# Performance work log

Measured on AMD Instinct MI355X. Metric: run time of the kernel, lower is better.

Reference implementation:

```python
import jax, jax.numpy as jnp
import numpy as np

N_NODES = 50000
N_EDGES = 800000
IN_DIM = 32
EMBED_DIM = 64
OUT_DIM = 1
N_LAYERS = 8


def setup_inputs() -> dict:
    key = jax.random.key(0)
    ks = jax.random.split(key, 10)
    x = jax.random.normal(ks[0], (N_NODES, IN_DIM), dtype=jnp.float32)
    src = jax.random.randint(ks[1], (N_EDGES,), 0, N_NODES, dtype=jnp.int32)
    dst = jax.random.randint(ks[2], (N_EDGES,), 0, N_NODES, dtype=jnp.int32)
    # learned params
    s_in = 1.0 / np.sqrt(IN_DIM)
    s_d = 1.0 / np.sqrt(EMBED_DIM)
    W_embed = jax.random.uniform(ks[3], (IN_DIM, EMBED_DIM), jnp.float32, -s_in, s_in)
    b_embed = jnp.zeros((EMBED_DIM,), jnp.float32)
    Ws = jax.random.uniform(ks[4], (N_LAYERS, EMBED_DIM, EMBED_DIM), jnp.float32, -s_d, s_d)
    bs = jnp.zeros((N_LAYERS, EMBED_DIM), jnp.float32)
    W_dec = jax.random.uniform(ks[5], (EMBED_DIM, OUT_DIM), jnp.float32, -s_d, s_d)
    b_dec = jnp.zeros((OUT_DIM,), jnp.float32)
    return {"x": x, "src": src, "dst": dst, "W_embed": W_embed, "b_embed": b_embed,
            "Ws": Ws, "bs": bs, "W_dec": W_dec, "b_dec": b_dec}


def reference(x, src, dst, W_embed, b_embed, Ws, bs, W_dec, b_dec):
    N = x.shape[0]
    ones = jnp.ones(src.shape[0], x.dtype)
    # DGL GraphConv norm='both': degrees clamped to min 1
    deg_out = jnp.maximum(jax.ops.segment_sum(ones, src, num_segments=N), 1.0)
    deg_in = jnp.maximum(jax.ops.segment_sum(ones, dst, num_segments=N), 1.0)
    inv_out = deg_out ** -0.5  # [N]
    inv_in = deg_in ** -0.5    # [N]

    h = x @ W_embed + b_embed  # [N, D]

    def layer(h, wb):
        W, b = wb
        m = (h * inv_out[:, None])[src]                      # gather [E, D]
        agg = jax.ops.segment_sum(m, dst, num_segments=N)    # scatter-add [N, D]
        h = (agg * inv_in[:, None]) @ W + b
        return h, None

    h, _ = jax.lax.scan(layer, h, (Ws, bs))
    return h @ W_dec + b_dec  # [N, OUT_DIM]
```

## Files before the change

kernel.cpp:

```cpp
#include <hip/hip_runtime.h>


#define PAD 48
#define HS 32
#define HR 4
#define HBLK (HS * HR)

__global__ __launch_bounds__(256) void prep_hist_kernel(
        const int* __restrict__ src,
        const float* __restrict__ W_embed, const float* __restrict__ b_embed,
        const float* __restrict__ Ws, const float* __restrict__ bs,
        const float* __restrict__ W_dec, float* __restrict__ coef,
        int* __restrict__ cursor, unsigned* __restrict__ pu, int N, int E) {
    __shared__ unsigned lds[8192];
    int b = blockIdx.x;
    if (b < HBLK) {
        int q = b >> 2, r = b & 3;
        for (int i = threadIdx.x; i < 8192; i += 256) lds[i] = 0;
        __syncthreads();
        int base = r << 14;
        int per = ((E + HS - 1) / HS + 3) & ~3;
        int e0 = q * per;
        int e1 = e0 + per; if (e1 > E) e1 = E;
        if (e0 < e1) {
            const int4* p4 = (const int4*)(src + e0);
            int m4 = (e1 - e0) >> 2;
            for (int i = threadIdx.x; i < m4; i += 256) {
                int4 v = p4[i];
                int t;
                t = v.x - base; if ((unsigned)t < 16384u) atomicAdd(&lds[t >> 1], 1u << ((t & 1) * 16));
                t = v.y - base; if ((unsigned)t < 16384u) atomicAdd(&lds[t >> 1], 1u << ((t & 1) * 16));
                t = v.z - base; if ((unsigned)t < 16384u) atomicAdd(&lds[t >> 1], 1u << ((t & 1) * 16));
                t = v.w - base; if ((unsigned)t < 16384u) atomicAdd(&lds[t >> 1], 1u << ((t & 1) * 16));
            }
            for (int e = e0 + (m4 << 2) + threadIdx.x; e < e1; e += 256) {
                int t = src[e] - base;
                if ((unsigned)t < 16384u) atomicAdd(&lds[t >> 1], 1u << ((t & 1) * 16));
            }
        }
        __syncthreads();
        unsigned* outp = pu + (size_t)b * 8192;
        for (int i = threadIdx.x; i < 8192; i += 256) outp[i] = lds[i];
    } else if (b == HBLK) {
        __shared__ float shv[64];
        __shared__ float shg[9];
        int i = threadIdx.x;
        if (i < 64) shv[i] = W_dec[i];
        __syncthreads();
        for (int l = 7; l >= 0; --l) {
            float a = 0.f;
            if (i < 64) {
                float p = bs[l * 64 + i] * shv[i];
                for (int d = 32; d; d >>= 1) p += __shfl_xor(p, d);
                if (i == 0) shg[l + 1] = p;
                const float* Wrow = Ws + l * 4096 + i * 64;
                for (int j = 0; j < 64; ++j) a += Wrow[j] * shv[j];
            }
            __syncthreads();
            if (i < 64) shv[i] = a;
            __syncthreads();
        }
        if (i < 64) {
            float p = b_embed[i] * shv[i];
            for (int d = 32; d; d >>= 1) p += __shfl_xor(p, d);
            if (i == 0) shg[0] = p;
        }
        __syncthreads();
        if (i < 32) {
            float a = 0.f;
            const float* Wr = W_embed + i * 64;
            for (int j = 0; j < 64; ++j) a += Wr[j] * shv[j];
            coef[16 + i] = a;
        }
        if (i < 9) coef[i] = shg[i];
    } else {
        int g = (b - HBLK - 1) * 256 + threadIdx.x;
        int stride = (gridDim.x - HBLK - 1) * 256;
        for (int i = g; i < N; i += stride) cursor[i] = 0;
    }
}

__global__ __launch_bounds__(256) void fill_kernel(
        const int* __restrict__ src, const int* __restrict__ dst,
        int* __restrict__ cursor, unsigned short* __restrict__ csr, int E) {
    int i = blockIdx.x * 256 + threadIdx.x;
    if (i >= E) return;
    int s = src[i], d = dst[i];
    int p = atomicAdd(&cursor[d], 1);
    if (p < PAD) csr[(size_t)d * PAD + p] = (unsigned short)s;
}

__global__ __launch_bounds__(256) void z0_kernel(
        const float* __restrict__ x, const float* __restrict__ coef,
        const unsigned* __restrict__ pu, const int* __restrict__ cursor,
        float* __restrict__ inv_out, float* __restrict__ inv_in,
        float* __restrict__ ts0, int N) {
    __shared__ float w[33];
    if (threadIdx.x < 32) w[threadIdx.x] = coef[16 + threadIdx.x];
    if (threadIdx.x == 32) w[32] = coef[0];
    __syncthreads();
    int n = blockIdx.x * 256 + threadIdx.x;
    if (n >= N) return;
    const float4* xr = (const float4*)(x + (size_t)n * 32);
    float acc = 0.f;
#pragma unroll
    for (int q = 0; q < 8; ++q) {
        float4 vv = xr[q];
        acc += vv.x * w[q * 4] + vv.y * w[q * 4 + 1] + vv.z * w[q * 4 + 2] + vv.w * w[q * 4 + 3];
    }
    int r = n >> 14, j = (n & 16383) >> 1, sh = (n & 1) * 16;
    int co = 0;
#pragma unroll
    for (int q = 0; q < HS; ++q)
        co += (pu[(size_t)((q << 2) | r) * 8192 + j] >> sh) & 0xFFFF;
    if (co < 1) co = 1;
    int ci = cursor[n]; if (ci < 1) ci = 1;
    float io = rsqrtf((float)co);
    inv_out[n] = io;
    inv_in[n] = rsqrtf((float)ci);
    ts0[n] = io * (acc + w[32]);
}

__device__ __forceinline__ float quad_gather(const unsigned short* __restrict__ row,
                                             const float* __restrict__ ta,
                                             int c, int sub) {
    float acc = 0.f;
#pragma unroll
    for (int t = 0; t < PAD / 16; ++t) {
        int eb = sub * 4 + 16 * t;
        if (eb < c) {
            uint2 v = *(const uint2*)(row + eb);
            unsigned i0 = v.x & 0xFFFF, i1 = v.x >> 16;
            unsigned i2 = v.y & 0xFFFF, i3 = v.y >> 16;
            acc += ta[i0];
            if (eb + 1 < c) acc += ta[i1];
            if (eb + 2 < c) acc += ta[i2];
            if (eb + 3 < c) acc += ta[i3];
        }
    }
    return acc;
}

__global__ __launch_bounds__(256) void prop_kernel(
        const float* __restrict__ ts_in, float* __restrict__ ts_out,
        const float* __restrict__ inv_out, const float* __restrict__ inv_in,
        const int* __restrict__ cursor, const unsigned short* __restrict__ csr,
        const float* __restrict__ coef, int k, int N) {
    int tid = blockIdx.x * 256 + threadIdx.x;
    int n = tid >> 2, sub = tid & 3;
    if (n >= N) return;
    int c = cursor[n]; if (c > PAD) c = PAD;
    float acc = quad_gather(csr + (size_t)n * PAD, ts_in, c, sub);
    acc += __shfl_xor(acc, 1);
    acc += __shfl_xor(acc, 2);
    if (sub == 0) ts_out[n] = inv_out[n] * (inv_in[n] * acc + coef[k]);
}

__global__ __launch_bounds__(256) void final_kernel(
        const float* __restrict__ ts_in, float* __restrict__ out,
        const float* __restrict__ inv_in, const int* __restrict__ cursor,
        const unsigned short* __restrict__ csr, const float* __restrict__ coef,
        const float* __restrict__ b_dec, int N) {
    int tid = blockIdx.x * 256 + threadIdx.x;
    int n = tid >> 2, sub = tid & 3;
    if (n >= N) return;
    int c = cursor[n]; if (c > PAD) c = PAD;
    float acc = quad_gather(csr + (size_t)n * PAD, ts_in, c, sub);
    acc += __shfl_xor(acc, 1);
    acc += __shfl_xor(acc, 2);
    if (sub == 0) out[n] = inv_in[n] * acc + coef[8] + b_dec[0];
}

__global__ __launch_bounds__(256) void prep_kernel_i(
        const float* __restrict__ W_embed, const float* __restrict__ b_embed,
        const float* __restrict__ Ws, const float* __restrict__ bs,
        const float* __restrict__ W_dec, float* __restrict__ coef,
        int* __restrict__ cnt, int NZ) {
    int g = blockIdx.x * 256 + threadIdx.x;
    for (int i = g; i < NZ; i += gridDim.x * 256) cnt[i] = 0;
    if (blockIdx.x == 0) {
        __shared__ float shv[64];
        __shared__ float shg[9];
        int i = threadIdx.x;
        if (i < 64) shv[i] = W_dec[i];
        __syncthreads();
        for (int l = 7; l >= 0; --l) {
            float a = 0.f;
            if (i < 64) {
                float p = bs[l * 64 + i] * shv[i];
                for (int d = 32; d; d >>= 1) p += __shfl_xor(p, d);
                if (i == 0) shg[l + 1] = p;
                const float* Wrow = Ws + l * 4096 + i * 64;
                for (int j = 0; j < 64; ++j) a += Wrow[j] * shv[j];
            }
            __syncthreads();
            if (i < 64) shv[i] = a;
            __syncthreads();
        }
        if (i < 64) {
            float p = b_embed[i] * shv[i];
            for (int d = 32; d; d >>= 1) p += __shfl_xor(p, d);
            if (i == 0) shg[0] = p;
        }
        __syncthreads();
        if (i < 32) {
            float a = 0.f;
            const float* Wr = W_embed + i * 64;
            for (int j = 0; j < 64; ++j) a += Wr[j] * shv[j];
            coef[16 + i] = a;
        }
        if (i < 9) coef[i] = shg[i];
    }
}

__global__ __launch_bounds__(256) void fill_kernel_i(
        const int* __restrict__ src, const int* __restrict__ dst,
        int* __restrict__ cnt_out, int* __restrict__ cursor,
        int* __restrict__ csr, int E) {
    int i = blockIdx.x * 256 + threadIdx.x;
    if (i >= E) return;
    int s = src[i], d = dst[i];
    atomicAdd(&cnt_out[s], 1);
    int p = atomicAdd(&cursor[d], 1);
    if (p < PAD) csr[(size_t)d * PAD + p] = s;
}

__global__ __launch_bounds__(256) void z0_kernel_i(
        const float* __restrict__ x, const float* __restrict__ coef,
        const int* __restrict__ cnt_out, const int* __restrict__ cursor,
        float* __restrict__ inv_out, float* __restrict__ inv_in,
        float* __restrict__ ts0, int N) {
    __shared__ float w[33];
    if (threadIdx.x < 32) w[threadIdx.x] = coef[16 + threadIdx.x];
    if (threadIdx.x == 32) w[32] = coef[0];
    __syncthreads();
    int n = blockIdx.x * 256 + threadIdx.x;
    if (n >= N) return;
    const float4* xr = (const float4*)(x + (size_t)n * 32);
    float acc = 0.f;
#pragma unroll
    for (int q = 0; q < 8; ++q) {
        float4 vv = xr[q];
        acc += vv.x * w[q * 4] + vv.y * w[q * 4 + 1] + vv.z * w[q * 4 + 2] + vv.w * w[q * 4 + 3];
    }
    int co = cnt_out[n]; if (co < 1) co = 1;
    int ci = cursor[n];  if (ci < 1) ci = 1;
    float io = rsqrtf((float)co);
    inv_out[n] = io;
    inv_in[n] = rsqrtf((float)ci);
    ts0[n] = io * (acc + w[32]);
}

__global__ __launch_bounds__(256) void prop_kernel_i(
        const float* __restrict__ ts_in, float* __restrict__ ts_out,
        const float* __restrict__ inv_out, const float* __restrict__ inv_in,
        const int* __restrict__ cursor, const int* __restrict__ csr,
        const float* __restrict__ coef, int k, int N) {
    int n = blockIdx.x * 256 + threadIdx.x;
    if (n >= N) return;
    int c = cursor[n]; if (c > PAD) c = PAD;
    const int* row = csr + (size_t)n * PAD;
    float acc = 0.f;
    for (int e = 0; e < c; ++e) acc += ts_in[row[e]];
    ts_out[n] = inv_out[n] * (inv_in[n] * acc + coef[k]);
}

__global__ __launch_bounds__(256) void final_kernel_i(
        const float* __restrict__ ts_in, float* __restrict__ out,
        const float* __restrict__ inv_in, const int* __restrict__ cursor,
        const int* __restrict__ csr, const float* __restrict__ coef,
        const float* __restrict__ b_dec, int N) {
    int n = blockIdx.x * 256 + threadIdx.x;
    if (n >= N) return;
    int c = cursor[n]; if (c > PAD) c = PAD;
    const int* row = csr + (size_t)n * PAD;
    float acc = 0.f;
    for (int e = 0; e < c; ++e) acc += ts_in[row[e]];
    out[n] = inv_in[n] * acc + coef[8] + b_dec[0];
}

extern "C" void kernel_launch(void* const* d_in, const int* in_sizes, int n_in,
                              void* d_out, int out_size, void* d_ws, size_t ws_size,
                              hipStream_t stream) {
    const float* x       = (const float*)d_in[0];
    const int*   src     = (const int*)d_in[1];
    const int*   dst     = (const int*)d_in[2];
    const float* W_embed = (const float*)d_in[3];
    const float* b_embed = (const float*)d_in[4];
    const float* Ws      = (const float*)d_in[5];
    const float* bs      = (const float*)d_in[6];
    const float* W_dec   = (const float*)d_in[7];
    const float* b_dec   = (const float*)d_in[8];
    float* out = (float*)d_out;
    int N = in_sizes[0] / 32;
    int E = in_sizes[1];

    char* w = (char*)d_ws;
    size_t o = 0;
    int* cursor = (int*)(w + o); o += (size_t)N * 4;
    size_t region = (size_t)HBLK * 8192 * 4;
    if ((size_t)N * 4 > region) region = (size_t)N * 4;
    unsigned* pu  = (unsigned*)(w + o);
    int* cnt_out  = (int*)(w + o);
    o += region; o = (o + 255) & ~(size_t)255;
    float* inv_out = (float*)(w + o); o += (size_t)N * 4; o = (o + 255) & ~(size_t)255;
    float* inv_in  = (float*)(w + o); o += (size_t)N * 4; o = (o + 255) & ~(size_t)255;
    float* coef    = (float*)(w + o); o += 256;
    float* tsA     = (float*)(w + o); o += (size_t)N * 4; o = (o + 255) & ~(size_t)255;
    float* tsB     = (float*)(w + o); o += (size_t)N * 4; o = (o + 255) & ~(size_t)255;
    void* csr_mem  = (void*)(w + o);

    int nbl  = (N + 255) / 256;
    int nbl4 = (4 * N + 255) / 256;
    int ebl  = (E + 255) / 256;

    if (N <= 65536) {
        unsigned short* csr = (unsigned short*)csr_mem;
        prep_hist_kernel<<<HBLK + 1 + 31, 256, 0, stream>>>(src, W_embed, b_embed, Ws, bs,
                                                            W_dec, coef, cursor, pu, N, E);
        fill_kernel<<<ebl, 256, 0, stream>>>(src, dst, cursor, csr, E);
        z0_kernel<<<nbl, 256, 0, stream>>>(x, coef, pu, cursor, inv_out, inv_in, tsA, N);
        float* ta = tsA; float* tb = tsB;
        for (int k = 1; k <= 7; ++k) {
            prop_kernel<<<nbl4, 256, 0, stream>>>(ta, tb, inv_out, inv_in, cursor, csr, coef, k, N);
            float* tmp = ta; ta = tb; tb = tmp;
        }
        final_kernel<<<nbl4, 256, 0, stream>>>(ta, out, inv_in, cursor, csr, coef, b_dec, N);
    } else {
        int* csr = (int*)csr_mem;
        prep_kernel_i<<<128, 256, 0, stream>>>(W_embed, b_embed, Ws, bs, W_dec, coef, cursor, 2 * N);
        fill_kernel_i<<<ebl, 256, 0, stream>>>(src, dst, cnt_out, cursor, csr, E);
        z0_kernel_i<<<nbl, 256, 0, stream>>>(x, coef, cnt_out, cursor, inv_out, inv_in, tsA, N);
        float* ta = tsA; float* tb = tsB;
        for (int k = 1; k <= 7; ++k) {
            prop_kernel_i<<<nbl, 256, 0, stream>>>(ta, tb, inv_out, inv_in, cursor, csr, coef, k, N);
            float* tmp = ta; ta = tb; tb = tmp;
        }
        final_kernel_i<<<nbl, 256, 0, stream>>>(ta, out, inv_in, cursor, csr, coef, b_dec, N);
    }
}
```

Baseline: 118.3 us.

## Replace global-atomic CSR fill with LDS-histogram based per-range slot assignment

```diff
diff --git a/kernel.cpp b/kernel.cpp
--- a/kernel.cpp
+++ b/kernel.cpp
@@ -2,46 +2,55 @@
 
 
 #define PAD 48
-#define HS 32
-#define HR 4
-#define HBLK (HS * HR)
+#define RS  8192
+#define RH  (RS / 2)
+#define QS  8
+#define QF  16
 
 __global__ __launch_bounds__(256) void prep_hist_kernel(
-        const int* __restrict__ src,
+        const int* __restrict__ src, const int* __restrict__ dst,
         const float* __restrict__ W_embed, const float* __restrict__ b_embed,
         const float* __restrict__ Ws, const float* __restrict__ bs,
         const float* __restrict__ W_dec, float* __restrict__ coef,
-        int* __restrict__ cursor, unsigned* __restrict__ pu, int N, int E) {
-    __shared__ unsigned lds[8192];
+        unsigned* __restrict__ pu_src, unsigned* __restrict__ pu_dst,
+        int NR, int N, int E) {
+    __shared__ unsigned lds[RH];
     int b = blockIdx.x;
-    if (b < HBLK) {
-        int q = b >> 2, r = b & 3;
-        for (int i = threadIdx.x; i < 8192; i += 256) lds[i] = 0;
-        __syncthreads();
-        int base = r << 14;
-        int per = ((E + HS - 1) / HS + 3) & ~3;
+    int nsrc = NR * QS;
+    int nhist = nsrc + NR * QF;
+    if (b < nhist) {
+        bool is_src = b < nsrc;
+        int bb = is_src ? b : b - nsrc;
+        int r = bb % NR, q = bb / NR;
+        int Q = is_src ? QS : QF;
+        const int* __restrict__ arr = is_src ? src : dst;
+        unsigned* __restrict__ pu = is_src ? pu_src : pu_dst;
+        for (int i = threadIdx.x; i < RH; i += 256) lds[i] = 0;
+        __syncthreads();
+        int base = r * RS;
+        int per = ((E + Q - 1) / Q + 3) & ~3;
         int e0 = q * per;
         int e1 = e0 + per; if (e1 > E) e1 = E;
-        if (e0 < e1) {
-            const int4* p4 = (const int4*)(src + e0);
+        if (e0 < E) {
+            const int4* p4 = (const int4*)(arr + e0);
             int m4 = (e1 - e0) >> 2;
             for (int i = threadIdx.x; i < m4; i += 256) {
                 int4 v = p4[i];
                 int t;
-                t = v.x - base; if ((unsigned)t < 16384u) atomicAdd(&lds[t >> 1], 1u << ((t & 1) * 16));
-                t = v.y - base; if ((unsigned)t < 16384u) atomicAdd(&lds[t >> 1], 1u << ((t & 1) * 16));
-                t = v.z - base; if ((unsigned)t < 16384u) atomicAdd(&lds[t >> 1], 1u << ((t & 1) * 16));
-                t = v.w - base; if ((unsigned)t < 16384u) atomicAdd(&lds[t >> 1], 1u << ((t & 1) * 16));
+                t = v.x - base; if ((unsigned)t < (unsigned)RS) atomicAdd(&lds[t >> 1], 1u << ((t & 1) * 16));
+                t = v.y - base; if ((unsigned)t < (unsigned)RS) atomicAdd(&lds[t >> 1], 1u << ((t & 1) * 16));
+                t = v.z - base; if ((unsigned)t < (unsigned)RS) atomicAdd(&lds[t >> 1], 1u << ((t & 1) * 16));
+                t = v.w - base; if ((unsigned)t < (unsigned)RS) atomicAdd(&lds[t >> 1], 1u << ((t & 1) * 16));
             }
             for (int e = e0 + (m4 << 2) + threadIdx.x; e < e1; e += 256) {
-                int t = src[e] - base;
-                if ((unsigned)t < 16384u) atomicAdd(&lds[t >> 1], 1u << ((t & 1) * 16));
-            }
-        }
-        __syncthreads();
-        unsigned* outp = pu + (size_t)b * 8192;
-        for (int i = threadIdx.x; i < 8192; i += 256) outp[i] = lds[i];
-    } else if (b == HBLK) {
+                int t = arr[e] - base;
+                if ((unsigned)t < (unsigned)RS) atomicAdd(&lds[t >> 1], 1u << ((t & 1) * 16));
+            }
+        }
+        __syncthreads();
+        unsigned* outp = pu + (size_t)(q * NR + r) * RH;
+        for (int i = threadIdx.x; i < RH; i += 256) outp[i] = lds[i];
+    } else if (b == nhist) {
         __shared__ float shv[64];
         __shared__ float shg[9];
         int i = threadIdx.x;
@@ -73,28 +82,79 @@
             coef[16 + i] = a;
         }
         if (i < 9) coef[i] = shg[i];
-    } else {
-        int g = (b - HBLK - 1) * 256 + threadIdx.x;
-        int stride = (gridDim.x - HBLK - 1) * 256;
-        for (int i = g; i < N; i += stride) cursor[i] = 0;
     }
 }
 
 __global__ __launch_bounds__(256) void fill_kernel(
         const int* __restrict__ src, const int* __restrict__ dst,
-        int* __restrict__ cursor, unsigned short* __restrict__ csr, int E) {
-    int i = blockIdx.x * 256 + threadIdx.x;
-    if (i >= E) return;
-    int s = src[i], d = dst[i];
-    int p = atomicAdd(&cursor[d], 1);
-    if (p < PAD) csr[(size_t)d * PAD + p] = (unsigned short)s;
+        const unsigned* __restrict__ pu_dst, unsigned* __restrict__ cnt_in,
+        unsigned short* __restrict__ csr, int NR, int E) {
+    __shared__ unsigned cur[RH];
+    int b = blockIdx.x;
+    int r = b % NR, q = b / NR;
+    for (int j = threadIdx.x; j < RH; j += 256) {
+        unsigned s = 0;
+        for (int qq = 0; qq < q; ++qq) s += pu_dst[(size_t)(qq * NR + r) * RH + j];
+        cur[j] = s;
+    }
+    __syncthreads();
+    int base = r * RS;
+    int per = ((E + QF - 1) / QF + 3) & ~3;
+    int e0 = q * per;
+    int e1 = e0 + per; if (e1 > E) e1 = E;
+    if (e0 < E) {
+        const int4* s4p = (const int4*)(src + e0);
+        const int4* d4p = (const int4*)(dst + e0);
+        int m4 = (e1 - e0) >> 2;
+        for (int i = threadIdx.x; i < m4; i += 256) {
+            int4 sv = s4p[i];
+            int4 dv = d4p[i];
+            int t, sh, p; unsigned old;
+            t = dv.x - base;
+            if ((unsigned)t < (unsigned)RS) {
+                sh = (t & 1) * 16; old = atomicAdd(&cur[t >> 1], 1u << sh);
+                p = (old >> sh) & 0xFFFF;
+                if (p < PAD) csr[(size_t)(base + t) * PAD + p] = (unsigned short)sv.x;
+            }
+            t = dv.y - base;
+            if ((unsigned)t < (unsigned)RS) {
+                sh = (t & 1) * 16; old = atomicAdd(&cur[t >> 1], 1u << sh);
+                p = (old >> sh) & 0xFFFF;
+                if (p < PAD) csr[(size_t)(base + t) * PAD + p] = (unsigned short)sv.y;
+            }
+            t = dv.z - base;
+            if ((unsigned)t < (unsigned)RS) {
+                sh = (t & 1) * 16; old = atomicAdd(&cur[t >> 1], 1u << sh);
+                p = (old >> sh) & 0xFFFF;
+                if (p < PAD) csr[(size_t)(base + t) * PAD + p] = (unsigned short)sv.z;
+            }
+            t = dv.w - base;
+            if ((unsigned)t < (unsigned)RS) {
+                sh = (t & 1) * 16; old = atomicAdd(&cur[t >> 1], 1u << sh);
+                p = (old >> sh) & 0xFFFF;
+                if (p < PAD) csr[(size_t)(base + t) * PAD + p] = (unsigned short)sv.w;
+            }
+        }
+        for (int e = e0 + (m4 << 2) + threadIdx.x; e < e1; e += 256) {
+            int t = dst[e] - base;
+            if ((unsigned)t < (unsigned)RS) {
+                int sh = (t & 1) * 16;
+                unsigned old = atomicAdd(&cur[t >> 1], 1u << sh);
+                int p = (old >> sh) & 0xFFFF;
+                if (p < PAD) csr[(size_t)(base + t) * PAD + p] = (unsigned short)src[e];
+            }
+        }
+    }
+    __syncthreads();
+    if (q == QF - 1)
+        for (int j = threadIdx.x; j < RH; j += 256) cnt_in[(size_t)r * RH + j] = cur[j];
 }
 
 __global__ __launch_bounds__(256) void z0_kernel(
         const float* __restrict__ x, const float* __restrict__ coef,
-        const unsigned* __restrict__ pu, const int* __restrict__ cursor,
+        const unsigned* __restrict__ pu_src, const unsigned* __restrict__ cnt_in,
         float* __restrict__ inv_out, float* __restrict__ inv_in,
-        float* __restrict__ ts0, int N) {
+        float* __restrict__ ts0, int NR, int N) {
     __shared__ float w[33];
     if (threadIdx.x < 32) w[threadIdx.x] = coef[16 + threadIdx.x];
     if (threadIdx.x == 32) w[32] = coef[0];
@@ -108,13 +168,14 @@
         float4 vv = xr[q];
         acc += vv.x * w[q * 4] + vv.y * w[q * 4 + 1] + vv.z * w[q * 4 + 2] + vv.w * w[q * 4 + 3];
     }
-    int r = n >> 14, j = (n & 16383) >> 1, sh = (n & 1) * 16;
+    int r = n >> 13, j = (n & (RS - 1)) >> 1, sh = (n & 1) * 16;
     int co = 0;
 #pragma unroll
-    for (int q = 0; q < HS; ++q)
-        co += (pu[(size_t)((q << 2) | r) * 8192 + j] >> sh) & 0xFFFF;
+    for (int q = 0; q < QS; ++q)
+        co += (pu_src[(size_t)(q * NR + r) * RH + j] >> sh) & 0xFFFF;
     if (co < 1) co = 1;
-    int ci = cursor[n]; if (ci < 1) ci = 1;
+    int ci = (cnt_in[n >> 1] >> sh) & 0xFFFF;
+    if (ci < 1) ci = 1;
     float io = rsqrtf((float)co);
     inv_out[n] = io;
     inv_in[n] = rsqrtf((float)ci);
@@ -144,12 +205,13 @@
 __global__ __launch_bounds__(256) void prop_kernel(
         const float* __restrict__ ts_in, float* __restrict__ ts_out,
         const float* __restrict__ inv_out, const float* __restrict__ inv_in,
-        const int* __restrict__ cursor, const unsigned short* __restrict__ csr,
+        const unsigned* __restrict__ cnt_in, const unsigned short* __restrict__ csr,
         const float* __restrict__ coef, int k, int N) {
     int tid = blockIdx.x * 256 + threadIdx.x;
     int n = tid >> 2, sub = tid & 3;
     if (n >= N) return;
-    int c = cursor[n]; if (c > PAD) c = PAD;
+    int c = (cnt_in[n >> 1] >> ((n & 1) * 16)) & 0xFFFF;
+    if (c > PAD) c = PAD;
     float acc = quad_gather(csr + (size_t)n * PAD, ts_in, c, sub);
     acc += __shfl_xor(acc, 1);
     acc += __shfl_xor(acc, 2);
@@ -158,13 +220,14 @@
 
 __global__ __launch_bounds__(256) void final_kernel(
         const float* __restrict__ ts_in, float* __restrict__ out,
-        const float* __restrict__ inv_in, const int* __restrict__ cursor,
+        const float* __restrict__ inv_in, const unsigned* __restrict__ cnt_in,
         const unsigned short* __restrict__ csr, const float* __restrict__ coef,
         const float* __restrict__ b_dec, int N) {
     int tid = blockIdx.x * 256 + threadIdx.x;
     int n = tid >> 2, sub = tid & 3;
     if (n >= N) return;
-    int c = cursor[n]; if (c > PAD) c = PAD;
+    int c = (cnt_in[n >> 1] >> ((n & 1) * 16)) & 0xFFFF;
+    if (c > PAD) c = PAD;
     float acc = quad_gather(csr + (size_t)n * PAD, ts_in, c, sub);
     acc += __shfl_xor(acc, 1);
     acc += __shfl_xor(acc, 2);
@@ -295,39 +358,47 @@
     int N = in_sizes[0] / 32;
     int E = in_sizes[1];
 
-    char* w = (char*)d_ws;
-    size_t o = 0;
-    int* cursor = (int*)(w + o); o += (size_t)N * 4;
-    size_t region = (size_t)HBLK * 8192 * 4;
-    if ((size_t)N * 4 > region) region = (size_t)N * 4;
-    unsigned* pu  = (unsigned*)(w + o);
-    int* cnt_out  = (int*)(w + o);
-    o += region; o = (o + 255) & ~(size_t)255;
-    float* inv_out = (float*)(w + o); o += (size_t)N * 4; o = (o + 255) & ~(size_t)255;
-    float* inv_in  = (float*)(w + o); o += (size_t)N * 4; o = (o + 255) & ~(size_t)255;
-    float* coef    = (float*)(w + o); o += 256;
-    float* tsA     = (float*)(w + o); o += (size_t)N * 4; o = (o + 255) & ~(size_t)255;
-    float* tsB     = (float*)(w + o); o += (size_t)N * 4; o = (o + 255) & ~(size_t)255;
-    void* csr_mem  = (void*)(w + o);
-
     int nbl  = (N + 255) / 256;
     int nbl4 = (4 * N + 255) / 256;
     int ebl  = (E + 255) / 256;
+    char* w = (char*)d_ws;
 
     if (N <= 65536) {
-        unsigned short* csr = (unsigned short*)csr_mem;
-        prep_hist_kernel<<<HBLK + 1 + 31, 256, 0, stream>>>(src, W_embed, b_embed, Ws, bs,
-                                                            W_dec, coef, cursor, pu, N, E);
-        fill_kernel<<<ebl, 256, 0, stream>>>(src, dst, cursor, csr, E);
-        z0_kernel<<<nbl, 256, 0, stream>>>(x, coef, pu, cursor, inv_out, inv_in, tsA, N);
+        int NR = (N + RS - 1) / RS;
+        size_t o = 0;
+        unsigned* pu_src = (unsigned*)(w + o); o += (size_t)NR * QS * RH * 4;
+        unsigned* pu_dst = (unsigned*)(w + o); o += (size_t)NR * QF * RH * 4;
+        unsigned* cnt_in = (unsigned*)(w + o); o += (size_t)NR * RH * 4;
+        o = (o + 255) & ~(size_t)255;
+        float* inv_out = (float*)(w + o); o += (size_t)N * 4; o = (o + 255) & ~(size_t)255;
+        float* inv_in  = (float*)(w + o); o += (size_t)N * 4; o = (o + 255) & ~(size_t)255;
+        float* coef    = (float*)(w + o); o += 256;
+        float* tsA     = (float*)(w + o); o += (size_t)N * 4; o = (o + 255) & ~(size_t)255;
+        float* tsB     = (float*)(w + o); o += (size_t)N * 4; o = (o + 255) & ~(size_t)255;
+        unsigned short* csr = (unsigned short*)(w + o);
+
+        prep_hist_kernel<<<NR * (QS + QF) + 1, 256, 0, stream>>>(
+            src, dst, W_embed, b_embed, Ws, bs, W_dec, coef, pu_src, pu_dst, NR, N, E);
+        fill_kernel<<<NR * QF, 256, 0, stream>>>(src, dst, pu_dst, cnt_in, csr, NR, E);
+        z0_kernel<<<nbl, 256, 0, stream>>>(x, coef, pu_src, cnt_in, inv_out, inv_in, tsA, NR, N);
         float* ta = tsA; float* tb = tsB;
         for (int k = 1; k <= 7; ++k) {
-            prop_kernel<<<nbl4, 256, 0, stream>>>(ta, tb, inv_out, inv_in, cursor, csr, coef, k, N);
+            prop_kernel<<<nbl4, 256, 0, stream>>>(ta, tb, inv_out, inv_in, cnt_in, csr, coef, k, N);
             float* tmp = ta; ta = tb; tb = tmp;
         }
-        final_kernel<<<nbl4, 256, 0, stream>>>(ta, out, inv_in, cursor, csr, coef, b_dec, N);
+        final_kernel<<<nbl4, 256, 0, stream>>>(ta, out, inv_in, cnt_in, csr, coef, b_dec, N);
     } else {
-        int* csr = (int*)csr_mem;
+        size_t o = 0;
+        int* cursor  = (int*)(w + o); o += (size_t)N * 4;
+        int* cnt_out = (int*)(w + o); o += (size_t)N * 4;
+        o = (o + 255) & ~(size_t)255;
+        float* inv_out = (float*)(w + o); o += (size_t)N * 4; o = (o + 255) & ~(size_t)255;
+        float* inv_in  = (float*)(w + o); o += (size_t)N * 4; o = (o + 255) & ~(size_t)255;
+        float* coef    = (float*)(w + o); o += 256;
+        float* tsA     = (float*)(w + o); o += (size_t)N * 4; o = (o + 255) & ~(size_t)255;
+        float* tsB     = (float*)(w + o); o += (size_t)N * 4; o = (o + 255) & ~(size_t)255;
+        int* csr = (int*)(w + o);
+
         prep_kernel_i<<<128, 256, 0, stream>>>(W_embed, b_embed, Ws, bs, W_dec, coef, cursor, 2 * N);
         fill_kernel_i<<<ebl, 256, 0, stream>>>(src, dst, cnt_out, cursor, csr, E);
         z0_kernel_i<<<nbl, 256, 0, stream>>>(x, coef, cnt_out, cursor, inv_out, inv_in, tsA, N);
```

Result: slower. 168.5 us (+42.4%).
